# Kernel optimization log

Hardware: AMD Instinct MI355X
Metric: run time of the kernel (lower is better)

## Reference

```python
import jax, jax.numpy as jnp
import numpy as np

EPS = float(np.finfo(np.float32).eps)
H = 256          # hidden_size
K = 10           # num_event_types
B, S = 32, 4096  # batch, seq_len


def _linear_params(kw, kb, fan_in, fan_out):
    # torch nn.Linear default init (uniform +-1/sqrt(fan_in)), then abs + clamp(min=eps)
    bound = 1.0 / np.sqrt(fan_in)
    w = jnp.clip(jnp.abs(jax.random.uniform(kw, (fan_out, fan_in), minval=-bound, maxval=bound, dtype=jnp.float32)), EPS)
    b = jnp.clip(jnp.abs(jax.random.uniform(kb, (fan_out,), minval=-bound, maxval=bound, dtype=jnp.float32)), EPS)
    return w, b


def setup_inputs() -> dict:
    key = jax.random.key(0)
    ks = jax.random.split(key, 12)
    w1, b1 = _linear_params(ks[0], ks[1], 1, H)        # layer_dense_1
    w2, b2 = _linear_params(ks[2], ks[3], 2 * H, H)    # layer_dense_2
    wA, bA = _linear_params(ks[4], ks[5], H, H)        # module_list[0]
    wB, bB = _linear_params(ks[6], ks[7], H, H)        # module_list[1]
    w3, b3 = _linear_params(ks[8], ks[9], H, K)        # layer_dense_3 linear
    hidden_states = jax.random.normal(ks[10], (B, S, H), dtype=jnp.float32)
    time_delta_seqs = jax.random.uniform(ks[11], (B, S), dtype=jnp.float32)
    return dict(hidden_states=hidden_states, time_delta_seqs=time_delta_seqs,
                w1=w1, b1=b1, w2=w2, b2=b2, wA=wA, bA=bA, wB=wB, bB=bB, w3=w3, b3=b3)


def _cumul_hazard(td, h, w1, b1, w2, b2, wA, bA, wB, bB, w3, b3):
    # layer_dense_1: Linear(1 -> H) on td[..., None]
    t = td[..., None] * w1[:, 0] + b1                      # [B,S,H]
    out = jnp.tanh(jnp.concatenate([h, t], axis=-1) @ w2.T + b2)  # [B,S,H]
    out = jnp.tanh(out @ wA.T + bA)
    out = jnp.tanh(out @ wB.T + bB)
    return jax.nn.softplus(out @ w3.T + b3)                # [B,S,K]


def reference(hidden_states, time_delta_seqs, w1, b1, w2, b2, wA, bA, wB, bB, w3, b3):
    f = lambda td: _cumul_hazard(td, hidden_states, w1, b1, w2, b2, wA, bA, wB, bB, w3, b3)
    # Each output element depends only on its own t[b,s] (elementwise in time),
    # so a single forward-mode JVP with tangent=ones yields the exact per-element
    # derivative for ALL event types at once (fuses torch's per-type grad loop).
    integral_lambda, d_dt = jax.jvp(f, (time_delta_seqs,), (jnp.ones_like(time_delta_seqs),))
    # torch takes grad of .mean() over [B,S], which scales the derivative by 1/(B*S)
    derivative_integral_lambda = d_dt / time_delta_seqs.size
    return integral_lambda, derivative_integral_lambda
```

## Files before the change

### kernel.cpp

```cpp
#include <hip/hip_runtime.h>
#include <hip/hip_bf16.h>
#include <stdint.h>

typedef __bf16 bf16x8 __attribute__((ext_vector_type(8)));
typedef __bf16 bf16x4 __attribute__((ext_vector_type(4)));
typedef float  f32x4  __attribute__((ext_vector_type(4)));
typedef float  f32x2  __attribute__((ext_vector_type(2)));

#define MFMA16(a,b,c) __builtin_amdgcn_mfma_f32_16x16x32_bf16((a),(b),(c),0,0,0)

static constexpr int H_   = 256;
static constexpr int KEV  = 10;
static constexpr int NTOK = 32 * 4096;

__device__ __forceinline__ float ptanh(float x){
    float t = x * x;
    float n = fmaf(t, t + 105.0f, 945.0f);
    float d = fmaf(t, fmaf(t, 15.0f, 420.0f), 945.0f);
    float r = x * n * __builtin_amdgcn_rcpf(d);
    return __builtin_amdgcn_fmed3f(r, -1.0f, 1.0f);
}

__device__ __forceinline__ bf16x8 cvtFrag(const float* p){
    f32x4 a = *(const f32x4*)p;
    f32x4 b = *(const f32x4*)(p + 4);
    bf16x8 r;
    #pragma unroll
    for (int j = 0; j < 4; ++j){ r[j] = (__bf16)a[j]; r[4 + j] = (__bf16)b[j]; }
    return r;
}

__global__ void prep_vc(const float* __restrict__ w1, const float* __restrict__ b1,
                        const float* __restrict__ w2, const float* __restrict__ b2,
                        const float* __restrict__ b3, float* __restrict__ vc){
    int j = blockIdx.x * 4 + (threadIdx.x >> 6);
    int l = threadIdx.x & 63;
    const float* row = w2 + (size_t)j * (2 * H_) + H_;
    float v = 0.f, cc = 0.f;
    #pragma unroll
    for (int i = 0; i < 4; ++i){
        int k = l + 64 * i;
        float w = row[k];
        v  += w * w1[k];
        cc += w * b1[k];
    }
    #pragma unroll
    for (int off = 32; off; off >>= 1){
        v  += __shfl_down(v,  off, 64);
        cc += __shfl_down(cc, off, 64);
    }
    if (l == 0){ vc[j] = v; vc[H_ + j] = cc + b2[j]; }
    if (blockIdx.x == 0 && threadIdx.x < 16)
        vc[2 * H_ + threadIdx.x] = (threadIdx.x < KEV) ? b3[threadIdx.x] : 0.0f;
}

__global__ void prep_pack(const float* __restrict__ w2, const float* __restrict__ wA,
                          const float* __restrict__ wB, const float* __restrict__ w3,
                          __hip_bfloat16* __restrict__ pk){
    int b  = blockIdx.x;
    int L  = b >> 4, n0 = b & 15;
    const float* W; int K, nrows;
    if (b == 48){ W = w3; K = H_; nrows = KEV; }
    else { W = (L == 0) ? w2 : ((L == 1) ? wA : wB); K = (L == 0) ? 2 * H_ : H_; nrows = 16; }
    __hip_bfloat16* dst = pk + (size_t)b * 4096;
    int t = threadIdx.x;
    #pragma unroll
    for (int u = 0; u < 2; ++u){
        int slot = t * 2 + u;
        int s = slot >> 6, q = (slot >> 4) & 3, c = slot & 15;
        int rr = (b == 48) ? c : (n0 * 16 + c);
        if (c < nrows){
            const float* src = W + (size_t)rr * K + 32 * s + 8 * q;
            #pragma unroll
            for (int j = 0; j < 8; ++j) dst[slot * 8 + j] = __float2bfloat16(src[j]);
        } else {
            #pragma unroll
            for (int j = 0; j < 8; ++j) dst[slot * 8 + j] = __float2bfloat16(0.0f);
        }
    }
}

__global__ __launch_bounds__(128, 3) void chfn_kernel(
    const float* __restrict__ hs, const float* __restrict__ td,
    const __hip_bfloat16* __restrict__ wpk,
    const float* __restrict__ bA, const float* __restrict__ bB,
    const float* __restrict__ vc,
    float* __restrict__ out)
{
    __shared__ __hip_bfloat16 sA[2 * 16 * H_];
    __shared__ __hip_bfloat16 sD[2 * 16 * H_];

    const int tid  = threadIdx.x;
    const int wave = tid >> 6;
    const int lane = tid & 63;
    const int q    = lane >> 4;
    const int c    = lane & 15;
    const int tb   = blockIdx.x * 32 + wave * 16;
    const int wrow = wave * 16;

    const bf16x8* wp = (const bf16x8*)wpk;
    const int ws = q * 16 + c;

    bf16x8 W0[8], W1[8];
    {
        const bf16x8* b = wp + ws;
        #pragma unroll
        for (int s = 0; s < 8; ++s) W0[s] = b[s * 64];
    }

    bf16x8 aF[8], aB[8];
    {
        const float* h0 = hs + (size_t)(tb + c) * H_ + 8 * q;
        #pragma unroll
        for (int s = 0; s < 8; ++s) aF[s] = cvtFrag(h0 + 32 * s);
    }
    float myTd = td[tb + c];

    #pragma unroll 2
    for (int n0 = 0; n0 < 16; ++n0){
        bf16x8* cur = (n0 & 1) ? W1 : W0;
        bf16x8* nxt = (n0 & 1) ? W0 : W1;
        {
            const bf16x8* b = wp + (size_t)(n0 + 1) * 512 + ws;
            #pragma unroll
            for (int s = 0; s < 8; ++s) nxt[s] = b[s * 64];
        }
        f32x4 v4 = *(const f32x4*)(vc + n0 * 16 + 4 * q);
        f32x4 c4 = *(const f32x4*)(vc + H_ + n0 * 16 + 4 * q);
        f32x4 fa = c4;
        f32x4 fb = {0.f,0.f,0.f,0.f};
        #pragma unroll
        for (int s = 0; s < 4; ++s){
            fa = MFMA16(cur[s],     aF[s],     fa);
            fb = MFMA16(cur[s + 4], aF[s + 4], fb);
        }
        bf16x4 pa, pd;
        #pragma unroll
        for (int r = 0; r < 4; ++r){
            float x  = fmaf(myTd, v4[r], fa[r] + fb[r]);
            float th = ptanh(x);
            float dd = fmaf(-th, th, 1.0f) * v4[r];
            pa[r] = (__bf16)th; pd[r] = (__bf16)dd;
        }
        int chn = 2 * n0 + (q >> 1);
        int off = (wrow + c) * H_ + (((chn + 4 * c) & 31) << 3) + ((q & 1) << 2);
        *(bf16x4*)((void*)(sA + off)) = pa;
        *(bf16x4*)((void*)(sD + off)) = pd;
    }

    #pragma unroll 1
    for (int L = 0; L < 2; ++L){
        const float* bias = L ? bB : bA;
        {
            const __hip_bfloat16* a0 = sA + (wrow + c) * H_;
            const __hip_bfloat16* d0 = sD + (wrow + c) * H_;
            #pragma unroll
            for (int s = 0; s < 8; ++s){
                int chn = (((4 * s + q) + 4 * c) & 31) << 3;
                aF[s] = *(const bf16x8*)(a0 + chn);
                aB[s] = *(const bf16x8*)(d0 + chn);
            }
        }
        #pragma unroll 2
        for (int n0 = 0; n0 < 16; ++n0){
            int g = 16 * (L + 1) + n0;
            bf16x8* cur = (n0 & 1) ? W1 : W0;
            bf16x8* nxt = (n0 & 1) ? W0 : W1;
            {
                const bf16x8* b = wp + (size_t)(g + 1) * 512 + ws;
                #pragma unroll
                for (int s = 0; s < 8; ++s) nxt[s] = b[s * 64];
            }
            f32x4 b4 = *(const f32x4*)(bias + n0 * 16 + 4 * q);
            f32x4 fa = b4;
            f32x4 fb = {0.f,0.f,0.f,0.f};
            f32x4 ga = {0.f,0.f,0.f,0.f};
            f32x4 gb = {0.f,0.f,0.f,0.f};
            #pragma unroll
            for (int s = 0; s < 4; ++s){
                fa = MFMA16(cur[s],     aF[s],     fa);
                ga = MFMA16(cur[s],     aB[s],     ga);
                fb = MFMA16(cur[s + 4], aF[s + 4], fb);
                gb = MFMA16(cur[s + 4], aB[s + 4], gb);
            }
            bf16x4 pa, pd;
            #pragma unroll
            for (int r = 0; r < 4; ++r){
                float th = ptanh(fa[r] + fb[r]);
                float dd = fmaf(-th, th, 1.0f) * (ga[r] + gb[r]);
                pa[r] = (__bf16)th; pd[r] = (__bf16)dd;
            }
            int chn = 2 * n0 + (q >> 1);
            int off = (wrow + c) * H_ + (((chn + 4 * c) & 31) << 3) + ((q & 1) << 2);
            *(bf16x4*)((void*)(sA + off)) = pa;
            *(bf16x4*)((void*)(sD + off)) = pd;
        }
    }

    {
        const __hip_bfloat16* a0 = sA + (wrow + c) * H_;
        const __hip_bfloat16* d0 = sD + (wrow + c) * H_;
        #pragma unroll
        for (int s = 0; s < 8; ++s){
            int chn = (((4 * s + q) + 4 * c) & 31) << 3;
            aF[s] = *(const bf16x8*)(a0 + chn);
            aB[s] = *(const bf16x8*)(d0 + chn);
        }
        bf16x8* cur = W0;
        f32x4 b4 = *(const f32x4*)(vc + 2 * H_ + 4 * q);
        f32x4 fa = b4;
        f32x4 fb = {0.f,0.f,0.f,0.f};
        f32x4 ga = {0.f,0.f,0.f,0.f};
        f32x4 gb = {0.f,0.f,0.f,0.f};
        #pragma unroll
        for (int s = 0; s < 4; ++s){
            fa = MFMA16(cur[s],     aF[s],     fa);
            ga = MFMA16(cur[s],     aB[s],     ga);
            fb = MFMA16(cur[s + 4], aF[s + 4], fb);
            gb = MFMA16(cur[s + 4], aB[s + 4], gb);
        }
        int fbase = 4 * q;
        size_t token = tb + c;
        float sp[4], dv[4];
        #pragma unroll
        for (int r = 0; r < 4; ++r){
            float z  = fa[r] + fb[r];
            float a  = fabsf(z);
            float e  = __builtin_amdgcn_exp2f(-1.4426950408889634f * a);
            sp[r] = fmaxf(z, 0.f) + 0.69314718055994531f * __builtin_amdgcn_logf(1.0f + e);
            float sg = __builtin_amdgcn_rcpf(1.0f + e);
            sg = (z >= 0.f) ? sg : 1.0f - sg;
            dv[r] = sg * (ga[r] + gb[r]) * (1.0f / 131072.0f);
        }
        float* o0 = out + token * KEV + fbase;
        float* o1 = out + (size_t)NTOK * KEV + token * KEV + fbase;
        if (q < 2){
            *(f32x2*)o0       = (f32x2){sp[0], sp[1]};
            *(f32x2*)(o0 + 2) = (f32x2){sp[2], sp[3]};
            *(f32x2*)o1       = (f32x2){dv[0], dv[1]};
            *(f32x2*)(o1 + 2) = (f32x2){dv[2], dv[3]};
        } else if (q == 2){
            *(f32x2*)o0 = (f32x2){sp[0], sp[1]};
            *(f32x2*)o1 = (f32x2){dv[0], dv[1]};
        }
    }
}

extern "C" void kernel_launch(void* const* d_in, const int* in_sizes, int n_in,
                              void* d_out, int out_size, void* d_ws, size_t ws_size,
                              hipStream_t stream){
    const float* hs = (const float*)d_in[0];
    const float* td = (const float*)d_in[1];
    const float* w1 = (const float*)d_in[2];
    const float* b1 = (const float*)d_in[3];
    const float* w2 = (const float*)d_in[4];
    const float* b2 = (const float*)d_in[5];
    const float* wA = (const float*)d_in[6];
    const float* bA = (const float*)d_in[7];
    const float* wB = (const float*)d_in[8];
    const float* bB = (const float*)d_in[9];
    const float* w3 = (const float*)d_in[10];
    const float* b3 = (const float*)d_in[11];

    float*          vc  = (float*)d_ws;
    __hip_bfloat16* wpk = (__hip_bfloat16*)((char*)d_ws + 4096);
    float*          outp = (float*)d_out;

    prep_vc  <<<64, 256, 0, stream>>>(w1, b1, w2, b2, b3, vc);
    prep_pack<<<49, 256, 0, stream>>>(w2, wA, wB, w3, wpk);
    chfn_kernel<<<NTOK / 32, 128, 0, stream>>>(hs, td, wpk, bA, bB, vc, outp);
}
```

Before: 330.8 us.

## Stage weight chunks into LDS via async global_load_lds shared across 4 waves

Weight tiles are now streamed from global memory into a double-buffered shared-memory buffer using direct global-to-LDS loads, rather than each wave loading its own copy into registers. The block grows to 4 waves (64 tokens), so each weight chunk is fetched once per block and shared, which cuts global/L2 traffic and frees the register double-buffer. The activation LDS layout also gets an XOR swizzle to reduce bank conflicts. In exchange, every chunk step now needs a block-wide barrier, and the larger LDS footprint lowers occupancy.

Result: slower. 349.0 us (+5.5%).

```diff
diff --git a/kernel.cpp b/kernel.cpp
--- a/kernel.cpp
+++ b/kernel.cpp
@@ -80,33 +80,39 @@
     }
 }
 
-__global__ __launch_bounds__(128, 3) void chfn_kernel(
+typedef const __attribute__((address_space(1))) void* gvp;
+typedef __attribute__((address_space(3)))       void* lvp;
+
+__device__ __forceinline__ void stage_chunk(const __hip_bfloat16* wpk, __hip_bfloat16* buf,
+                                            int g, int wave, int lane){
+    const char* src = (const char*)wpk + (size_t)g * 8192 + wave * 2048 + lane * 16;
+    char*       dst = (char*)buf + wave * 2048;
+    __builtin_amdgcn_global_load_lds((gvp)(const void*)src,          (lvp)(void*)dst,          16, 0, 0);
+    __builtin_amdgcn_global_load_lds((gvp)(const void*)(src + 1024), (lvp)(void*)(dst + 1024), 16, 0, 0);
+}
+
+__global__ __launch_bounds__(256, 2) void chfn_kernel(
     const float* __restrict__ hs, const float* __restrict__ td,
     const __hip_bfloat16* __restrict__ wpk,
     const float* __restrict__ bA, const float* __restrict__ bB,
     const float* __restrict__ vc,
     float* __restrict__ out)
 {
-    __shared__ __hip_bfloat16 sA[2 * 16 * H_];
-    __shared__ __hip_bfloat16 sD[2 * 16 * H_];
+    __shared__ __hip_bfloat16 sW[2 * 4096];
+    __shared__ __hip_bfloat16 sA[4 * 16 * H_];
+    __shared__ __hip_bfloat16 sD[4 * 16 * H_];
 
     const int tid  = threadIdx.x;
     const int wave = tid >> 6;
     const int lane = tid & 63;
     const int q    = lane >> 4;
     const int c    = lane & 15;
-    const int tb   = blockIdx.x * 32 + wave * 16;
+    const int tb   = blockIdx.x * 64 + wave * 16;
     const int wrow = wave * 16;
-
-    const bf16x8* wp = (const bf16x8*)wpk;
-    const int ws = q * 16 + c;
-
-    bf16x8 W0[8], W1[8];
-    {
-        const bf16x8* b = wp + ws;
-        #pragma unroll
-        for (int s = 0; s < 8; ++s) W0[s] = b[s * 64];
-    }
+    const int xr   = (c >> 1) & 7;
+    const int ws   = q * 16 + c;
+
+    stage_chunk(wpk, sW, 0, wave, lane);
 
     bf16x8 aF[8], aB[8];
     {
@@ -116,14 +122,16 @@
     }
     float myTd = td[tb + c];
 
+    bf16x8 W[8];
+
     #pragma unroll 2
     for (int n0 = 0; n0 < 16; ++n0){
-        bf16x8* cur = (n0 & 1) ? W1 : W0;
-        bf16x8* nxt = (n0 & 1) ? W0 : W1;
+        __syncthreads();
+        stage_chunk(wpk, sW + ((n0 + 1) & 1) * 4096, n0 + 1, wave, lane);
         {
-            const bf16x8* b = wp + (size_t)(n0 + 1) * 512 + ws;
-            #pragma unroll
-            for (int s = 0; s < 8; ++s) nxt[s] = b[s * 64];
+            const bf16x8* b = (const bf16x8*)(sW + (n0 & 1) * 4096) + ws;
+            #pragma unroll
+            for (int s = 0; s < 8; ++s) W[s] = b[s * 64];
         }
         f32x4 v4 = *(const f32x4*)(vc + n0 * 16 + 4 * q);
         f32x4 c4 = *(const f32x4*)(vc + H_ + n0 * 16 + 4 * q);
@@ -131,8 +139,8 @@
         f32x4 fb = {0.f,0.f,0.f,0.f};
         #pragma unroll
         for (int s = 0; s < 4; ++s){
-            fa = MFMA16(cur[s],     aF[s],     fa);
-            fb = MFMA16(cur[s + 4], aF[s + 4], fb);
+            fa = MFMA16(W[s],     aF[s],     fa);
+            fb = MFMA16(W[s + 4], aF[s + 4], fb);
         }
         bf16x4 pa, pd;
         #pragma unroll
@@ -143,7 +151,7 @@
             pa[r] = (__bf16)th; pd[r] = (__bf16)dd;
         }
         int chn = 2 * n0 + (q >> 1);
-        int off = (wrow + c) * H_ + (((chn + 4 * c) & 31) << 3) + ((q & 1) << 2);
+        int off = (wrow + c) * H_ + ((((chn + 4 * c) & 31) ^ xr) << 3) + ((q & 1) << 2);
         *(bf16x4*)((void*)(sA + off)) = pa;
         *(bf16x4*)((void*)(sD + off)) = pd;
     }
@@ -156,20 +164,20 @@
             const __hip_bfloat16* d0 = sD + (wrow + c) * H_;
             #pragma unroll
             for (int s = 0; s < 8; ++s){
-                int chn = (((4 * s + q) + 4 * c) & 31) << 3;
-                aF[s] = *(const bf16x8*)(a0 + chn);
-                aB[s] = *(const bf16x8*)(d0 + chn);
+                int g8 = ((((4 * s + q) + 4 * c) & 31) ^ xr) << 3;
+                aF[s] = *(const bf16x8*)(a0 + g8);
+                aB[s] = *(const bf16x8*)(d0 + g8);
             }
         }
         #pragma unroll 2
         for (int n0 = 0; n0 < 16; ++n0){
             int g = 16 * (L + 1) + n0;
-            bf16x8* cur = (n0 & 1) ? W1 : W0;
-            bf16x8* nxt = (n0 & 1) ? W0 : W1;
+            __syncthreads();
+            stage_chunk(wpk, sW + ((g + 1) & 1) * 4096, g + 1, wave, lane);
             {
-                const bf16x8* b = wp + (size_t)(g + 1) * 512 + ws;
+                const bf16x8* b = (const bf16x8*)(sW + (g & 1) * 4096) + ws;
                 #pragma unroll
-                for (int s = 0; s < 8; ++s) nxt[s] = b[s * 64];
+                for (int s = 0; s < 8; ++s) W[s] = b[s * 64];
             }
             f32x4 b4 = *(const f32x4*)(bias + n0 * 16 + 4 * q);
             f32x4 fa = b4;
@@ -178,10 +186,10 @@
             f32x4 gb = {0.f,0.f,0.f,0.f};
             #pragma unroll
             for (int s = 0; s < 4; ++s){
-                fa = MFMA16(cur[s],     aF[s],     fa);
-                ga = MFMA16(cur[s],     aB[s],     ga);
-                fb = MFMA16(cur[s + 4], aF[s + 4], fb);
-                gb = MFMA16(cur[s + 4], aB[s + 4], gb);
+                fa = MFMA16(W[s],     aF[s],     fa);
+                ga = MFMA16(W[s],     aB[s],     ga);
+                fb = MFMA16(W[s + 4], aF[s + 4], fb);
+                gb = MFMA16(W[s + 4], aB[s + 4], gb);
             }
             bf16x4 pa, pd;
             #pragma unroll
@@ -191,22 +199,27 @@
                 pa[r] = (__bf16)th; pd[r] = (__bf16)dd;
             }
             int chn = 2 * n0 + (q >> 1);
-            int off = (wrow + c) * H_ + (((chn + 4 * c) & 31) << 3) + ((q & 1) << 2);
+            int off = (wrow + c) * H_ + ((((chn + 4 * c) & 31) ^ xr) << 3) + ((q & 1) << 2);
             *(bf16x4*)((void*)(sA + off)) = pa;
             *(bf16x4*)((void*)(sD + off)) = pd;
         }
     }
 
     {
+        __syncthreads();
+        {
+            const bf16x8* b = (const bf16x8*)sW + ws;
+            #pragma unroll
+            for (int s = 0; s < 8; ++s) W[s] = b[s * 64];
+        }
         const __hip_bfloat16* a0 = sA + (wrow + c) * H_;
         const __hip_bfloat16* d0 = sD + (wrow + c) * H_;
         #pragma unroll
         for (int s = 0; s < 8; ++s){
-            int chn = (((4 * s + q) + 4 * c) & 31) << 3;
-            aF[s] = *(const bf16x8*)(a0 + chn);
-            aB[s] = *(const bf16x8*)(d0 + chn);
-        }
-        bf16x8* cur = W0;
+            int g8 = ((((4 * s + q) + 4 * c) & 31) ^ xr) << 3;
+            aF[s] = *(const bf16x8*)(a0 + g8);
+            aB[s] = *(const bf16x8*)(d0 + g8);
+        }
         f32x4 b4 = *(const f32x4*)(vc + 2 * H_ + 4 * q);
         f32x4 fa = b4;
         f32x4 fb = {0.f,0.f,0.f,0.f};
@@ -214,10 +227,10 @@
         f32x4 gb = {0.f,0.f,0.f,0.f};
         #pragma unroll
         for (int s = 0; s < 4; ++s){
-            fa = MFMA16(cur[s],     aF[s],     fa);
-            ga = MFMA16(cur[s],     aB[s],     ga);
-            fb = MFMA16(cur[s + 4], aF[s + 4], fb);
-            gb = MFMA16(cur[s + 4], aB[s + 4], gb);
+            fa = MFMA16(W[s],     aF[s],     fa);
+            ga = MFMA16(W[s],     aB[s],     ga);
+            fb = MFMA16(W[s + 4], aF[s + 4], fb);
+            gb = MFMA16(W[s + 4], aB[s + 4], gb);
         }
         int fbase = 4 * q;
         size_t token = tb + c;
@@ -268,5 +281,5 @@
 
     prep_vc  <<<64, 256, 0, stream>>>(w1, b1, w2, b2, b3, vc);
     prep_pack<<<49, 256, 0, stream>>>(w2, wA, wB, w3, wpk);
-    chfn_kernel<<<NTOK / 32, 128, 0, stream>>>(hs, td, wpk, bA, bB, vc, outp);
-}
+    chfn_kernel<<<NTOK / 64, 256, 0, stream>>>(hs, td, wpk, bA, bB, vc, outp);
+}
```
